# Optimization experiments

Hardware: AMD Instinct MI355X
Metric: run time of the kernel (lower is better)

The kernel has to match this reference:

```python
import jax, jax.numpy as jnp
import numpy as np

B, S, IN, OUT = 4, 2048, 4096, 11008


def setup_inputs() -> dict:
    key = jax.random.key(0)
    k1, k2, k3, k4, k5 = jax.random.split(key, 5)
    x = jax.random.normal(k1, (B, S, IN), dtype=jnp.float32)
    # int8 quantized weights, stored as int32 per harness spec but values in int8 range
    W_int8 = jax.random.randint(k2, (OUT, IN), -128, 128, dtype=jnp.int32)
    # per-output-channel scales (small positive) and zero-points
    scale = jax.random.uniform(k3, (OUT,), dtype=jnp.float32, minval=1e-3, maxval=2e-2)
    zero = jax.random.uniform(k4, (OUT,), dtype=jnp.float32, minval=-8.0, maxval=8.0)
    bias = jax.random.normal(k5, (OUT,), dtype=jnp.float32) * 0.01
    return {"x": x, "W_int8": W_int8, "scale": scale, "zero": zero, "bias": bias}


def reference(x, W_int8, scale, zero, bias):
    # Original torch forward raises on NaN/Inf in x; for valid inputs the math is
    # quant_matmul: dequantize W = (W_int8 - zero) * scale (per output channel),
    # then y = x @ W.T + bias.
    W = (W_int8.astype(jnp.float32) - zero[:, None]) * scale[:, None]  # [OUT, IN]
    y = jnp.einsum('bsi,oi->bso', x, W) + bias  # [B, S, OUT]
    return y
```

## Files before the change

kernel.cpp:

```cpp
#include <hip/hip_runtime.h>
#include <stdint.h>


#define M_DIM 8192
#define N_DIM 11008
#define K_DIM 4096
#define NT    (K_DIM / 128)
#define BUFB  65536

typedef __attribute__((ext_vector_type(4))) int i32x4;


__global__ void convert_w_kernel(const int* __restrict__ w,
                                 int8_t* __restrict__ o, int n4) {
  int idx = blockIdx.x * blockDim.x + threadIdx.x;
  int stride = gridDim.x * blockDim.x;
  for (int i = idx; i < n4; i += stride) {
    int4 v = ((const int4*)w)[i];
    int r = (v.x & 255) | ((v.y & 255) << 8) | ((v.z & 255) << 16) | ((v.w & 255) << 24);
    ((int*)o)[i] = r;
  }
}

__global__ __launch_bounds__(256) void quantx_kernel(
    const float* __restrict__ x, int8_t* __restrict__ h8, int8_t* __restrict__ l8,
    float* __restrict__ xs, float* __restrict__ rsum) {
  const int row = blockIdx.x;
  const int t = threadIdx.x;
  const float4* px = (const float4*)(x + (size_t)row * K_DIM);
  float4 v[4];
  float mx = 0.f, sm = 0.f;
  #pragma unroll
  for (int i = 0; i < 4; ++i) {
    v[i] = px[i * 256 + t];
    mx = fmaxf(mx, fmaxf(fmaxf(fabsf(v[i].x), fabsf(v[i].y)),
                         fmaxf(fabsf(v[i].z), fabsf(v[i].w))));
    sm += v[i].x + v[i].y + v[i].z + v[i].w;
  }
  #pragma unroll
  for (int off = 32; off > 0; off >>= 1) {
    mx = fmaxf(mx, __shfl_down(mx, off));
    sm += __shfl_down(sm, off);
  }
  __shared__ float rmx[4], rsm[4];
  const int wv = t >> 6, ln = t & 63;
  if (ln == 0) { rmx[wv] = mx; rsm[wv] = sm; }
  __syncthreads();
  const float rowmax = fmaxf(fmaxf(rmx[0], rmx[1]), fmaxf(rmx[2], rmx[3]));
  if (t == 0) {
    xs[row] = rowmax > 0.f ? rowmax / 16256.f : 0.f;
    rsum[row] = rsm[0] + rsm[1] + rsm[2] + rsm[3];
  }
  const float inv = rowmax > 0.f ? 16256.f / rowmax : 0.f;
  int* hp = (int*)(h8 + (size_t)row * K_DIM);
  int* lp = (int*)(l8 + (size_t)row * K_DIM);
  #pragma unroll
  for (int i = 0; i < 4; ++i) {
    int q0 = (int)rintf(v[i].x * inv);
    int q1 = (int)rintf(v[i].y * inv);
    int q2 = (int)rintf(v[i].z * inv);
    int q3 = (int)rintf(v[i].w * inv);
    int h0 = (q0 + 64) >> 7, h1 = (q1 + 64) >> 7, h2 = (q2 + 64) >> 7, h3 = (q3 + 64) >> 7;
    int l0 = q0 - (h0 << 7), l1 = q1 - (h1 << 7), l2 = q2 - (h2 << 7), l3 = q3 - (h3 << 7);
    hp[i * 256 + t] = (h0 & 255) | ((h1 & 255) << 8) | ((h2 & 255) << 16) | ((h3 & 255) << 24);
    lp[i * 256 + t] = (l0 & 255) | ((l1 & 255) << 8) | ((l2 & 255) << 16) | ((l3 & 255) << 24);
  }
}


__device__ __forceinline__ void stage_tile(
    const int8_t* __restrict__ Ah, const int8_t* __restrict__ Al,
    const int8_t* __restrict__ Bw, size_t a_base, size_t b_base,
    int ks, int srow, int scol, int wave, int8_t* buf) {
  #pragma unroll
  for (int r = 0; r < 2; ++r) {
    const int8_t* g = Ah + a_base + (size_t)(r * 64 + srow) * K_DIM + ks + scol;
    __builtin_amdgcn_global_load_lds((const __attribute__((address_space(1))) void*)g,
        (__attribute__((address_space(3))) void*)(buf + r * 8192 + wave * 1024), 16, 0, 0);
  }
  #pragma unroll
  for (int r = 0; r < 2; ++r) {
    const int8_t* g = Al + a_base + (size_t)(r * 64 + srow) * K_DIM + ks + scol;
    __builtin_amdgcn_global_load_lds((const __attribute__((address_space(1))) void*)g,
        (__attribute__((address_space(3))) void*)(buf + 16384 + r * 8192 + wave * 1024), 16, 0, 0);
  }
  #pragma unroll
  for (int r = 0; r < 4; ++r) {
    const int8_t* g = Bw + b_base + (size_t)(r * 64 + srow) * K_DIM + ks + scol;
    __builtin_amdgcn_global_load_lds((const __attribute__((address_space(1))) void*)g,
        (__attribute__((address_space(3))) void*)(buf + 32768 + r * 8192 + wave * 1024), 16, 0, 0);
  }
}

__global__ __launch_bounds__(512, 2) void qgemm_kernel(
    const int8_t* __restrict__ Ah, const int8_t* __restrict__ Al,
    const int8_t* __restrict__ Bw, const float* __restrict__ xs,
    const float* __restrict__ rowsum, const float* __restrict__ scale,
    const float* __restrict__ zero, const float* __restrict__ bias,
    float* __restrict__ out) {
  extern __shared__ int8_t smem[];

  const int tid = threadIdx.x;
  const int wave = tid >> 6;
  const int lane = tid & 63;

  const int bid = blockIdx.x;
  const int wg = (bid & 7) * 344 + (bid >> 3);
  const int group = wg / 344;
  const int rem = wg % 344;
  const int bm = group * 8 + (rem & 7);
  const int bn = rem >> 3;

  const int wr = wave >> 2;
  const int wc = wave & 3;

  i32x4 acch[4][4], accl[4][4];
  #pragma unroll
  for (int i = 0; i < 4; ++i)
    #pragma unroll
    for (int j = 0; j < 4; ++j) {
      acch[i][j] = (i32x4){0, 0, 0, 0};
      accl[i][j] = (i32x4){0, 0, 0, 0};
    }

  const int srow = tid >> 3;
  const int scol = (((tid & 7) ^ ((tid >> 3) & 7)) << 4);
  const size_t a_base = (size_t)(bm * 128) * K_DIM;
  const size_t b_base = (size_t)((size_t)bn * 256) * K_DIM;

  const int fr = lane & 15;
  const int g = lane >> 4;
  const int sw = fr & 7;
  const int sc0 = ((g ^ sw) << 4);
  const int sc1 = (((g + 4) ^ sw) << 4);

  stage_tile(Ah, Al, Bw, a_base, b_base, 0, srow, scol, wave, smem);
  asm volatile("s_waitcnt vmcnt(0)" ::: "memory");
  asm volatile("s_barrier" ::: "memory");

  for (int t = 0; t < NT; ++t) {
    if (t + 1 < NT) {
      stage_tile(Ah, Al, Bw, a_base, b_base, (t + 1) * 128, srow, scol, wave,
                 smem + ((t + 1) & 1) * BUFB);
      asm volatile("s_waitcnt vmcnt(8)" ::: "memory");
    } else {
      asm volatile("s_waitcnt vmcnt(0)" ::: "memory");
    }
    asm volatile("s_barrier" ::: "memory");

    const int8_t* buf = smem + (t & 1) * BUFB;
    const int8_t* ldsAh_ = buf;
    const int8_t* ldsAl_ = buf + 16384;
    const int8_t* ldsB_  = buf + 32768;

    #pragma unroll
    for (int h = 0; h < 2; ++h) {
      const int sc = h ? sc1 : sc0;
      i32x4 bfrag[4];
      #pragma unroll
      for (int ni = 0; ni < 4; ++ni) {
        const int row = wc * 64 + ni * 16 + fr;
        bfrag[ni] = *(const i32x4*)(ldsB_ + row * 128 + sc);
      }
      #pragma unroll
      for (int mi = 0; mi < 4; ++mi) {
        const int arow = (wr * 64 + mi * 16 + fr) * 128 + sc;
        i32x4 ahf = *(const i32x4*)(ldsAh_ + arow);
        i32x4 alf = *(const i32x4*)(ldsAl_ + arow);
        #pragma unroll
        for (int ni = 0; ni < 4; ++ni) {
          acch[mi][ni] = __builtin_amdgcn_mfma_i32_16x16x64_i8(ahf, bfrag[ni], acch[mi][ni], 0, 0, 0);
          accl[mi][ni] = __builtin_amdgcn_mfma_i32_16x16x64_i8(alf, bfrag[ni], accl[mi][ni], 0, 0, 0);
        }
      }
    }
    asm volatile("s_barrier" ::: "memory");
  }

  const int row0 = bm * 128 + wr * 64;
  const int col0 = bn * 256 + wc * 64;
  float s_[4], sz_[4], b_[4];
  #pragma unroll
  for (int ni = 0; ni < 4; ++ni) {
    const int n = col0 + ni * 16 + fr;
    const float s = scale[n];
    s_[ni] = s;
    sz_[ni] = s * zero[n];
    b_[ni] = bias[n];
  }
  #pragma unroll
  for (int mi = 0; mi < 4; ++mi) {
    #pragma unroll
    for (int j = 0; j < 4; ++j) {
      const int m = row0 + mi * 16 + g * 4 + j;
      const float xsm = xs[m];
      const float rs = rowsum[m];
      float* po = out + (size_t)m * N_DIM + col0;
      #pragma unroll
      for (int ni = 0; ni < 4; ++ni) {
        const float G = xsm * (128.f * (float)acch[mi][ni][j] + (float)accl[mi][ni][j]);
        po[ni * 16 + fr] = s_[ni] * G - sz_[ni] * rs + b_[ni];
      }
    }
  }
}


__global__ void fallback_kernel(const float* __restrict__ x, const int* __restrict__ w,
                                const float* __restrict__ scale, const float* __restrict__ zero,
                                const float* __restrict__ bias, float* __restrict__ out) {
  const int n = blockIdx.x * 16 + (threadIdx.x & 15);
  const int m = blockIdx.y * 16 + (threadIdx.x >> 4);
  const float z = zero[n];
  const float* xr = x + (size_t)m * K_DIM;
  const int* wr = w + (size_t)n * K_DIM;
  float acc = 0.f;
  for (int k = 0; k < K_DIM; ++k) acc += xr[k] * ((float)wr[k] - z);
  out[(size_t)m * N_DIM + n] = scale[n] * acc + bias[n];
}


extern "C" void kernel_launch(void* const* d_in, const int* in_sizes, int n_in,
                              void* d_out, int out_size, void* d_ws, size_t ws_size,
                              hipStream_t stream) {
  const float* x     = (const float*)d_in[0];
  const int*   w     = (const int*)d_in[1];
  const float* scale = (const float*)d_in[2];
  const float* zero  = (const float*)d_in[3];
  const float* bias  = (const float*)d_in[4];
  float* out = (float*)d_out;

  const size_t n_x = (size_t)M_DIM * K_DIM;
  const size_t n_w = (size_t)N_DIM * K_DIM;
  const size_t need = n_x * 2 + n_w + (size_t)M_DIM * 8;

  if (ws_size < need) {
    dim3 gr(N_DIM / 16, M_DIM / 16);
    fallback_kernel<<<gr, 256, 0, stream>>>(x, w, scale, zero, bias, out);
    return;
  }

  int8_t* x_h = (int8_t*)d_ws;
  int8_t* x_l = x_h + n_x;
  int8_t* w_8 = x_l + n_x;
  float* rsum = (float*)(w_8 + n_w);
  float* xs   = rsum + M_DIM;

  convert_w_kernel<<<2048, 256, 0, stream>>>(w, w_8, (int)(n_w / 4));
  quantx_kernel<<<M_DIM, 256, 0, stream>>>(x, x_h, x_l, xs, rsum);

  (void)hipFuncSetAttribute((const void*)qgemm_kernel,
                            hipFuncAttributeMaxDynamicSharedMemorySize, 2 * BUFB);

  const int nblocks = (M_DIM / 128) * (N_DIM / 256);
  qgemm_kernel<<<nblocks, 512, 2 * BUFB, stream>>>(x_h, x_l, w_8, xs, rsum,
                                                   scale, zero, bias, out);
}
```

Baseline: 738.0 us.

## Shrink int8 GEMM tile to 128x128 with K-step 64 and 4 waves

Restructures the int8 split-activation GEMM. Block tiles go from 128x256 with 8 waves and K-step 128 to 128x128 with 4 waves and K-step 64. Shared memory drops from 128KB dynamic to 48KB static, so more blocks fit per CU, and a new swizzle fits the 64-byte rows. The loop now issues the next-tile prefetch before the LDS reads, raises wave priority around the MFMA chain, and waits for all loads at the end of each iteration. The cost is lower arithmetic intensity per tile, twice as many blocks, and a barrier every 64 K elements.

```diff
diff --git a/kernel.cpp b/kernel.cpp
--- a/kernel.cpp
+++ b/kernel.cpp
@@ -5,8 +5,8 @@
 #define M_DIM 8192
 #define N_DIM 11008
 #define K_DIM 4096
-#define NT    (K_DIM / 128)
-#define BUFB  65536
+#define NT    (K_DIM / 64)
+#define BUFB  24576
 
 typedef __attribute__((ext_vector_type(4))) int i32x4;
 
@@ -73,46 +73,46 @@
     const int8_t* __restrict__ Bw, size_t a_base, size_t b_base,
     int ks, int srow, int scol, int wave, int8_t* buf) {
   #pragma unroll
-  for (int r = 0; r < 2; ++r) {
-    const int8_t* g = Ah + a_base + (size_t)(r * 64 + srow) * K_DIM + ks + scol;
+  for (int p = 0; p < 2; ++p) {
+    const int8_t* g = Ah + a_base + (size_t)(p * 64 + srow) * K_DIM + ks + scol;
     __builtin_amdgcn_global_load_lds((const __attribute__((address_space(1))) void*)g,
-        (__attribute__((address_space(3))) void*)(buf + r * 8192 + wave * 1024), 16, 0, 0);
-  }
-  #pragma unroll
-  for (int r = 0; r < 2; ++r) {
-    const int8_t* g = Al + a_base + (size_t)(r * 64 + srow) * K_DIM + ks + scol;
+        (__attribute__((address_space(3))) void*)(buf + p * 4096 + wave * 1024), 16, 0, 0);
+  }
+  #pragma unroll
+  for (int p = 0; p < 2; ++p) {
+    const int8_t* g = Al + a_base + (size_t)(p * 64 + srow) * K_DIM + ks + scol;
     __builtin_amdgcn_global_load_lds((const __attribute__((address_space(1))) void*)g,
-        (__attribute__((address_space(3))) void*)(buf + 16384 + r * 8192 + wave * 1024), 16, 0, 0);
-  }
-  #pragma unroll
-  for (int r = 0; r < 4; ++r) {
-    const int8_t* g = Bw + b_base + (size_t)(r * 64 + srow) * K_DIM + ks + scol;
+        (__attribute__((address_space(3))) void*)(buf + 8192 + p * 4096 + wave * 1024), 16, 0, 0);
+  }
+  #pragma unroll
+  for (int p = 0; p < 2; ++p) {
+    const int8_t* g = Bw + b_base + (size_t)(p * 64 + srow) * K_DIM + ks + scol;
     __builtin_amdgcn_global_load_lds((const __attribute__((address_space(1))) void*)g,
-        (__attribute__((address_space(3))) void*)(buf + 32768 + r * 8192 + wave * 1024), 16, 0, 0);
-  }
-}
-
-__global__ __launch_bounds__(512, 2) void qgemm_kernel(
+        (__attribute__((address_space(3))) void*)(buf + 16384 + p * 4096 + wave * 1024), 16, 0, 0);
+  }
+}
+
+__global__ __launch_bounds__(256, 2) void qgemm_kernel(
     const int8_t* __restrict__ Ah, const int8_t* __restrict__ Al,
     const int8_t* __restrict__ Bw, const float* __restrict__ xs,
     const float* __restrict__ rowsum, const float* __restrict__ scale,
     const float* __restrict__ zero, const float* __restrict__ bias,
     float* __restrict__ out) {
-  extern __shared__ int8_t smem[];
+  __shared__ int8_t smem[2 * BUFB];
 
   const int tid = threadIdx.x;
   const int wave = tid >> 6;
   const int lane = tid & 63;
 
   const int bid = blockIdx.x;
-  const int wg = (bid & 7) * 344 + (bid >> 3);
-  const int group = wg / 344;
-  const int rem = wg % 344;
+  const int wg = (bid & 7) * 688 + (bid >> 3);
+  const int group = wg / 688;
+  const int rem = wg % 688;
   const int bm = group * 8 + (rem & 7);
   const int bn = rem >> 3;
 
-  const int wr = wave >> 2;
-  const int wc = wave & 3;
+  const int wr = wave >> 1;
+  const int wc = wave & 1;
 
   i32x4 acch[4][4], accl[4][4];
   #pragma unroll
@@ -123,62 +123,64 @@
       accl[i][j] = (i32x4){0, 0, 0, 0};
     }
 
-  const int srow = tid >> 3;
-  const int scol = (((tid & 7) ^ ((tid >> 3) & 7)) << 4);
+  const int srow = tid >> 2;
+  const int scol = ((((tid & 3) - ((tid >> 3) & 3)) & 3) << 4);
   const size_t a_base = (size_t)(bm * 128) * K_DIM;
-  const size_t b_base = (size_t)((size_t)bn * 256) * K_DIM;
+  const size_t b_base = (size_t)(bn * 128) * K_DIM;
 
   const int fr = lane & 15;
   const int g = lane >> 4;
-  const int sw = fr & 7;
-  const int sc0 = ((g ^ sw) << 4);
-  const int sc1 = (((g + 4) ^ sw) << 4);
+  const int scA = (((g + (fr >> 1)) & 3) << 4);
+
+  int arow[4], brow[4];
+  #pragma unroll
+  for (int i = 0; i < 4; ++i) {
+    arow[i] = (wr * 64 + i * 16 + fr) * 64 + scA;
+    brow[i] = (wc * 64 + i * 16 + fr) * 64 + scA;
+  }
 
   stage_tile(Ah, Al, Bw, a_base, b_base, 0, srow, scol, wave, smem);
   asm volatile("s_waitcnt vmcnt(0)" ::: "memory");
-  asm volatile("s_barrier" ::: "memory");
-
+  __builtin_amdgcn_s_barrier();
+
+  #pragma unroll 1
   for (int t = 0; t < NT; ++t) {
-    if (t + 1 < NT) {
-      stage_tile(Ah, Al, Bw, a_base, b_base, (t + 1) * 128, srow, scol, wave,
-                 smem + ((t + 1) & 1) * BUFB);
-      asm volatile("s_waitcnt vmcnt(8)" ::: "memory");
-    } else {
-      asm volatile("s_waitcnt vmcnt(0)" ::: "memory");
+    const int8_t* buf = smem + (t & 1) * BUFB;
+    int8_t* nxt = smem + ((t + 1) & 1) * BUFB;
+    const int8_t* ldsAh_ = buf;
+    const int8_t* ldsAl_ = buf + 8192;
+    const int8_t* ldsB_  = buf + 16384;
+
+    if (t + 1 < NT)
+      stage_tile(Ah, Al, Bw, a_base, b_base, (t + 1) * 64, srow, scol, wave, nxt);
+
+    i32x4 af[4][2], bf[4];
+    #pragma unroll
+    for (int ni = 0; ni < 4; ++ni)
+      bf[ni] = *(const i32x4*)(ldsB_ + brow[ni]);
+    #pragma unroll
+    for (int mi = 0; mi < 4; ++mi) {
+      af[mi][0] = *(const i32x4*)(ldsAh_ + arow[mi]);
+      af[mi][1] = *(const i32x4*)(ldsAl_ + arow[mi]);
     }
-    asm volatile("s_barrier" ::: "memory");
-
-    const int8_t* buf = smem + (t & 1) * BUFB;
-    const int8_t* ldsAh_ = buf;
-    const int8_t* ldsAl_ = buf + 16384;
-    const int8_t* ldsB_  = buf + 32768;
-
-    #pragma unroll
-    for (int h = 0; h < 2; ++h) {
-      const int sc = h ? sc1 : sc0;
-      i32x4 bfrag[4];
+
+    __builtin_amdgcn_s_setprio(1);
+    #pragma unroll
+    for (int mi = 0; mi < 4; ++mi)
       #pragma unroll
       for (int ni = 0; ni < 4; ++ni) {
-        const int row = wc * 64 + ni * 16 + fr;
-        bfrag[ni] = *(const i32x4*)(ldsB_ + row * 128 + sc);
+        acch[mi][ni] = __builtin_amdgcn_mfma_i32_16x16x64_i8(af[mi][0], bf[ni], acch[mi][ni], 0, 0, 0);
+        accl[mi][ni] = __builtin_amdgcn_mfma_i32_16x16x64_i8(af[mi][1], bf[ni], accl[mi][ni], 0, 0, 0);
       }
-      #pragma unroll
-      for (int mi = 0; mi < 4; ++mi) {
-        const int arow = (wr * 64 + mi * 16 + fr) * 128 + sc;
-        i32x4 ahf = *(const i32x4*)(ldsAh_ + arow);
-        i32x4 alf = *(const i32x4*)(ldsAl_ + arow);
-        #pragma unroll
-        for (int ni = 0; ni < 4; ++ni) {
-          acch[mi][ni] = __builtin_amdgcn_mfma_i32_16x16x64_i8(ahf, bfrag[ni], acch[mi][ni], 0, 0, 0);
-          accl[mi][ni] = __builtin_amdgcn_mfma_i32_16x16x64_i8(alf, bfrag[ni], accl[mi][ni], 0, 0, 0);
-        }
-      }
-    }
-    asm volatile("s_barrier" ::: "memory");
+    __builtin_amdgcn_s_setprio(0);
+
+    asm volatile("s_waitcnt lgkmcnt(0)" ::: "memory");
+    asm volatile("s_waitcnt vmcnt(0)" ::: "memory");
+    __builtin_amdgcn_s_barrier();
   }
 
   const int row0 = bm * 128 + wr * 64;
-  const int col0 = bn * 256 + wc * 64;
+  const int col0 = bn * 128 + wc * 64;
   float s_[4], sz_[4], b_[4];
   #pragma unroll
   for (int ni = 0; ni < 4; ++ni) {
@@ -249,10 +251,7 @@
   convert_w_kernel<<<2048, 256, 0, stream>>>(w, w_8, (int)(n_w / 4));
   quantx_kernel<<<M_DIM, 256, 0, stream>>>(x, x_h, x_l, xs, rsum);
 
-  (void)hipFuncSetAttribute((const void*)qgemm_kernel,
-                            hipFuncAttributeMaxDynamicSharedMemorySize, 2 * BUFB);
-
-  const int nblocks = (M_DIM / 128) * (N_DIM / 256);
-  qgemm_kernel<<<nblocks, 512, 2 * BUFB, stream>>>(x_h, x_l, w_8, xs, rsum,
-                                                   scale, zero, bias, out);
-}
+  const int nblocks = (M_DIM / 128) * (N_DIM / 128);
+  qgemm_kernel<<<nblocks, 256, 0, stream>>>(x_h, x_l, w_8, xs, rsum,
+                                            scale, zero, bias, out);
+}
```

New measurement: 824.8 us. 1.12x slower.

## Software-pipeline LDS fragment reads with MFMA and interleave global prefetch

Applied to the files above, without the earlier changes.

Restructures the int8 GEMM main loop so the fragments for the first k-half of the next tile are read from LDS before the barrier ends the current iteration, and the second half is read while the first half's MFMAs run. Global-to-LDS prefetch of the next tile is split into A and B stages placed between the two MFMA groups, with scheduling barriers and s_setprio raising wave priority around the MFMA blocks. The loop now uses a single barrier per iteration instead of two. This aims to hide LDS and global load latency behind matrix ops. In exchange it holds two sets of fragment registers, which may raise register pressure and threaten the occupancy of 2 blocks per CU, and it waits on vmcnt(0) every iteration.

```diff
diff --git a/kernel.cpp b/kernel.cpp
--- a/kernel.cpp
+++ b/kernel.cpp
@@ -68,10 +68,9 @@
 }
 
 
-__device__ __forceinline__ void stage_tile(
+__device__ __forceinline__ void stage_A(
     const int8_t* __restrict__ Ah, const int8_t* __restrict__ Al,
-    const int8_t* __restrict__ Bw, size_t a_base, size_t b_base,
-    int ks, int srow, int scol, int wave, int8_t* buf) {
+    size_t a_base, int ks, int srow, int scol, int wave, int8_t* buf) {
   #pragma unroll
   for (int r = 0; r < 2; ++r) {
     const int8_t* g = Ah + a_base + (size_t)(r * 64 + srow) * K_DIM + ks + scol;
@@ -84,6 +83,11 @@
     __builtin_amdgcn_global_load_lds((const __attribute__((address_space(1))) void*)g,
         (__attribute__((address_space(3))) void*)(buf + 16384 + r * 8192 + wave * 1024), 16, 0, 0);
   }
+}
+
+__device__ __forceinline__ void stage_B(
+    const int8_t* __restrict__ Bw, size_t b_base,
+    int ks, int srow, int scol, int wave, int8_t* buf) {
   #pragma unroll
   for (int r = 0; r < 4; ++r) {
     const int8_t* g = Bw + b_base + (size_t)(r * 64 + srow) * K_DIM + ks + scol;
@@ -134,48 +138,81 @@
   const int sc0 = ((g ^ sw) << 4);
   const int sc1 = (((g + 4) ^ sw) << 4);
 
-  stage_tile(Ah, Al, Bw, a_base, b_base, 0, srow, scol, wave, smem);
+  int arow[4], brow[4];
+  #pragma unroll
+  for (int i = 0; i < 4; ++i) {
+    arow[i] = (wr * 64 + i * 16 + fr) * 128;
+    brow[i] = (wc * 64 + i * 16 + fr) * 128;
+  }
+
+#define RD(sc, ldsAh_, ldsAl_, ldsB_, af, bf) do {                       \
+    _Pragma("unroll")                                                    \
+    for (int ni = 0; ni < 4; ++ni)                                       \
+      bf[ni] = *(const i32x4*)((ldsB_) + brow[ni] + (sc));               \
+    _Pragma("unroll")                                                    \
+    for (int mi = 0; mi < 4; ++mi) {                                     \
+      af[mi][0] = *(const i32x4*)((ldsAh_) + arow[mi] + (sc));           \
+      af[mi][1] = *(const i32x4*)((ldsAl_) + arow[mi] + (sc));           \
+    }                                                                    \
+  } while (0)
+
+#define MM(af, bf) do {                                                  \
+    __builtin_amdgcn_s_setprio(1);                                       \
+    _Pragma("unroll")                                                    \
+    for (int mi = 0; mi < 4; ++mi)                                       \
+      _Pragma("unroll")                                                  \
+      for (int ni = 0; ni < 4; ++ni) {                                   \
+        acch[mi][ni] = __builtin_amdgcn_mfma_i32_16x16x64_i8(af[mi][0], bf[ni], acch[mi][ni], 0, 0, 0); \
+        accl[mi][ni] = __builtin_amdgcn_mfma_i32_16x16x64_i8(af[mi][1], bf[ni], accl[mi][ni], 0, 0, 0); \
+      }                                                                  \
+    __builtin_amdgcn_s_setprio(0);                                       \
+  } while (0)
+
+  i32x4 afA[4][2], bfA[4], afB[4][2], bfB[4];
+
+  stage_A(Ah, Al, a_base, 0, srow, scol, wave, smem);
+  stage_B(Bw, b_base, 0, srow, scol, wave, smem);
   asm volatile("s_waitcnt vmcnt(0)" ::: "memory");
-  asm volatile("s_barrier" ::: "memory");
-
+  __builtin_amdgcn_s_barrier();
+  {
+    const int8_t* b0 = smem;
+    RD(sc0, b0, b0 + 16384, b0 + 32768, afA, bfA);
+  }
+
+  #pragma unroll 1
   for (int t = 0; t < NT; ++t) {
-    if (t + 1 < NT) {
-      stage_tile(Ah, Al, Bw, a_base, b_base, (t + 1) * 128, srow, scol, wave,
-                 smem + ((t + 1) & 1) * BUFB);
-      asm volatile("s_waitcnt vmcnt(8)" ::: "memory");
-    } else {
-      asm volatile("s_waitcnt vmcnt(0)" ::: "memory");
-    }
-    asm volatile("s_barrier" ::: "memory");
-
     const int8_t* buf = smem + (t & 1) * BUFB;
+    int8_t* nxt = smem + ((t + 1) & 1) * BUFB;
     const int8_t* ldsAh_ = buf;
     const int8_t* ldsAl_ = buf + 16384;
     const int8_t* ldsB_  = buf + 32768;
-
-    #pragma unroll
-    for (int h = 0; h < 2; ++h) {
-      const int sc = h ? sc1 : sc0;
-      i32x4 bfrag[4];
-      #pragma unroll
-      for (int ni = 0; ni < 4; ++ni) {
-        const int row = wc * 64 + ni * 16 + fr;
-        bfrag[ni] = *(const i32x4*)(ldsB_ + row * 128 + sc);
-      }
-      #pragma unroll
-      for (int mi = 0; mi < 4; ++mi) {
-        const int arow = (wr * 64 + mi * 16 + fr) * 128 + sc;
-        i32x4 ahf = *(const i32x4*)(ldsAh_ + arow);
-        i32x4 alf = *(const i32x4*)(ldsAl_ + arow);
-        #pragma unroll
-        for (int ni = 0; ni < 4; ++ni) {
-          acch[mi][ni] = __builtin_amdgcn_mfma_i32_16x16x64_i8(ahf, bfrag[ni], acch[mi][ni], 0, 0, 0);
-          accl[mi][ni] = __builtin_amdgcn_mfma_i32_16x16x64_i8(alf, bfrag[ni], accl[mi][ni], 0, 0, 0);
-        }
-      }
+    const bool pf = (t + 1 < NT);
+    const int nks = (t + 1) * 128;
+
+    RD(sc1, ldsAh_, ldsAl_, ldsB_, afB, bfB);
+    __builtin_amdgcn_sched_barrier(0);
+    if (pf) stage_A(Ah, Al, a_base, nks, srow, scol, wave, nxt);
+
+    MM(afA, bfA);
+
+    if (pf) stage_B(Bw, b_base, nks, srow, scol, wave, nxt);
+    __builtin_amdgcn_sched_barrier(0);
+
+    MM(afB, bfB);
+
+    asm volatile("s_waitcnt vmcnt(0)" ::: "memory");
+    __builtin_amdgcn_s_barrier();
+
+    if (pf) {
+      const int8_t* nAh = nxt;
+      const int8_t* nAl = nxt + 16384;
+      const int8_t* nB  = nxt + 32768;
+      RD(sc0, nAh, nAl, nB, afA, bfA);
     }
-    asm volatile("s_barrier" ::: "memory");
-  }
+  }
+
+#undef RD
+#undef MM
 
   const int row0 = bm * 128 + wr * 64;
   const int col0 = bn * 256 + wc * 64;
```

After: 764.7 us. 1.04x slower.
